# Kernel tuning notes

Measured on AMD Instinct MI355X. Metric: run time of the kernel, lower is better.

The kernel has to match this reference:

```python
import jax, jax.numpy as jnp
import numpy as np

B, V_PREV, V_NEXT = 1, 16384, 65536
F_IN, F_OUT = 512, 256
NNZ_UP, N_EDGE = 65536, 524288
EPS = 1e-5


def batch_spmm(row, col, val, m, x):
    # sparse [m, n] (COO row/col/val) @ dense x [B, n, d] -> [B, m, d]
    contrib = val[None, :, None] * x[:, col, :]          # [B, nnz, d]
    return jnp.zeros((x.shape[0], m, x.shape[2]), x.dtype).at[:, row, :].add(contrib)


def batchnorm(x, g, b):
    # BatchNorm1d in training mode: stats over (batch, node) per channel
    mu = jnp.mean(x, axis=(0, 1), keepdims=True)
    var = jnp.var(x, axis=(0, 1), keepdims=True)
    return (x - mu) * jax.lax.rsqrt(var + EPS) * g + b


def ecc(x, src, dst, w, Ui_W, Ui_b, Uj_W, Uj_b):
    # edge-conditioned graph conv: out_i = Ui(x_i) + sum_{(j->i)} w_e * Uj(x_j)
    n_nodes = x.shape[1]
    uj = x @ Uj_W + Uj_b                                  # [B, V, Fout]
    msg = w[None, :, None] * uj[:, src, :]                # [B, E, Fout]
    agg = jnp.zeros((x.shape[0], n_nodes, Uj_W.shape[1]), x.dtype).at[:, dst, :].add(msg)
    return x @ Ui_W + Ui_b + agg


def setup_inputs() -> dict:
    key = jax.random.key(0)
    ks = jax.random.split(key, 16)
    s_in = 1.0 / np.sqrt(F_IN)
    s_out = 1.0 / np.sqrt(F_OUT)
    p = {}
    p["x"] = jax.random.normal(ks[0], (B, V_PREV, F_IN), jnp.float32)
    p["up_row"] = jnp.arange(NNZ_UP, dtype=jnp.int32)
    p["up_col"] = jax.random.randint(ks[1], (NNZ_UP,), 0, V_PREV)
    p["up_val"] = jax.random.uniform(ks[2], (NNZ_UP,), jnp.float32)
    p["edge_src"] = jax.random.randint(ks[3], (N_EDGE,), 0, V_NEXT)
    p["edge_dst"] = jax.random.randint(ks[4], (N_EDGE,), 0, V_NEXT)
    p["adj_val"] = jax.random.uniform(ks[5], (N_EDGE,), jnp.float32)
    p["W_res"] = jax.random.normal(ks[6], (F_IN, F_OUT), jnp.float32) * s_in
    p["b_res"] = jnp.zeros((F_OUT,), jnp.float32)
    p["bn0_g"] = jnp.ones((F_IN,), jnp.float32)
    p["bn0_b"] = jnp.zeros((F_IN,), jnp.float32)
    p["bn1_g"] = jnp.ones((F_OUT,), jnp.float32)
    p["bn1_b"] = jnp.zeros((F_OUT,), jnp.float32)
    p["Ui0_W"] = jax.random.normal(ks[7], (F_IN, F_OUT), jnp.float32) * s_in
    p["Ui0_b"] = jnp.zeros((F_OUT,), jnp.float32)
    p["Uj0_W"] = jax.random.normal(ks[8], (F_IN, F_OUT), jnp.float32) * s_in
    p["Uj0_b"] = jnp.zeros((F_OUT,), jnp.float32)
    p["Ui1_W"] = jax.random.normal(ks[9], (F_OUT, F_OUT), jnp.float32) * s_out
    p["Ui1_b"] = jnp.zeros((F_OUT,), jnp.float32)
    p["Uj1_W"] = jax.random.normal(ks[10], (F_OUT, F_OUT), jnp.float32) * s_out
    p["Uj1_b"] = jnp.zeros((F_OUT,), jnp.float32)
    return p


def reference(x, up_row, up_col, up_val, edge_src, edge_dst, adj_val,
              W_res, b_res, bn0_g, bn0_b, bn1_g, bn1_b,
              Ui0_W, Ui0_b, Uj0_W, Uj0_b, Ui1_W, Ui1_b, Uj1_W, Uj1_b):
    # residual branch: sparse upsample then 1x1 conv (= linear over channels)
    residual = batch_spmm(up_row, up_col, up_val, V_NEXT, x)      # [B, V_NEXT, F_IN]
    residual = residual @ W_res + b_res                           # [B, V_NEXT, F_OUT]
    # main branch
    out = jax.nn.relu(batchnorm(x, bn0_g, bn0_b))                 # [B, V_PREV, F_IN]
    out = batch_spmm(up_row, up_col, up_val, V_NEXT, out)         # [B, V_NEXT, F_IN]
    out = ecc(out, edge_src, edge_dst, adj_val, Ui0_W, Ui0_b, Uj0_W, Uj0_b)
    out = jax.nn.relu(batchnorm(out, bn1_g, bn1_b))
    out = ecc(out, edge_src, edge_dst, adj_val, Ui1_W, Ui1_b, Uj1_W, Uj1_b)
    return out + residual
```

## Files before the change

### kernel.cpp

```cpp
#include <hip/hip_runtime.h>

#define V_PREV 16384
#define V_NEXT 65536
#define F_IN   512
#define F_OUT  256
#define NNZ_UP 65536
#define N_EDGE 524288

using f32x4 = __attribute__((ext_vector_type(4))) float;
using bfrag = __attribute__((ext_vector_type(8))) short;

__device__ __forceinline__ ushort f2bf(float f) {
    union { float f; unsigned u; } v; v.f = f;
    unsigned r = (v.u + 0x7FFFu + ((v.u >> 16) & 1u)) >> 16;
    return (ushort)r;
}
__device__ __forceinline__ float bf2f(ushort h) {
    union { unsigned u; float f; } v; v.u = ((unsigned)h) << 16; return v.f;
}

__global__ void prep_all_kernel(const float* __restrict__ Wres,
                                const float* __restrict__ Ui0W, const float* __restrict__ Uj0W,
                                const float* __restrict__ Ui1W, const float* __restrict__ Uj1W,
                                const float* __restrict__ Ui1b, const float* __restrict__ bres,
                                const int* __restrict__ up_row, const int* __restrict__ up_col,
                                const float* __restrict__ up_val,
                                ushort* __restrict__ WresT, ushort* __restrict__ W0t,
                                ushort* __restrict__ W1cat, float* __restrict__ biasUi,
                                int* __restrict__ colof, float* __restrict__ valof,
                                int* __restrict__ zeroBase)
{
    int b = blockIdx.x, t = threadIdx.x;
    if (b < 1024) {
        int i = b * 256 + t;
        if (i < 256 * 512) {
            int n = i / 512, k = i % 512;
            WresT[i] = f2bf(Wres[k * 256 + n]);
            W1cat[i] = f2bf(k < 256 ? Ui1W[k * 256 + n] : Uj1W[(k - 256) * 256 + n]);
        }
        {
            int n = i / 512, k = i % 512;
            W0t[i] = f2bf(n < 256 ? Uj0W[k * 256 + n] : Ui0W[k * 256 + (n - 256)]);
        }
        if (i < 256) biasUi[i] = Ui1b[i] + bres[i];
    } else if (b < 1280) {
        int k = (b - 1024) * 256 + t;
        int r = up_row[k];
        colof[r] = up_col[k];
        valof[r] = up_val[k];
    } else {
        int i = (b - 1280) * 256 + t;
        zeroBase[i] = 0;
    }
}

__global__ void hist_bn0_kernel(const int* __restrict__ dst,
                                int* __restrict__ cnt,
                                const float* __restrict__ x,
                                float* __restrict__ psum0, float* __restrict__ psq0)
{
    int b = blockIdx.x, t = threadIdx.x;
    if (b < 2048) {
        int e = b * 256 + t;
        atomicAdd(&cnt[dst[e]], 1);
    } else {
        int blk = b - 2048;
        float s0 = 0, s1 = 0, q0 = 0, q1 = 0;
        for (int r = 0; r < 32; r++) {
            size_t base = ((size_t)blk * 32 + r) * 512;
            float a = x[base + t], bb = x[base + t + 256];
            s0 += a; q0 += a * a; s1 += bb; q1 += bb * bb;
        }
        psum0[blk * 512 + t] = s0; psum0[blk * 512 + t + 256] = s1;
        psq0 [blk * 512 + t] = q0; psq0 [blk * 512 + t + 256] = q1;
    }
}

__global__ void scan_block_kernel(const int* __restrict__ cnt, int* __restrict__ offs,
                                  int* __restrict__ bsum)
{
    __shared__ int buf[2][256];
    int t = threadIdx.x;
    int i = blockIdx.x * 256 + t;
    int v = cnt[i];
    int p = 0;
    buf[0][t] = v;
    __syncthreads();
    for (int d = 1; d < 256; d <<= 1) {
        int nv = buf[p][t] + ((t >= d) ? buf[p][t - d] : 0);
        buf[p ^ 1][t] = nv;
        p ^= 1;
        __syncthreads();
    }
    int incl = buf[p][t];
    offs[i] = incl - v;
    if (t == 255) bsum[blockIdx.x] = incl;
}

__global__ void add_offs_bnfin_kernel(int* __restrict__ offs, const int* __restrict__ bsum,
                                      int* __restrict__ cursor,
                                      const float* __restrict__ psum0, const float* __restrict__ psq0,
                                      const float* __restrict__ g0, const float* __restrict__ b0,
                                      float* __restrict__ sc0, float* __restrict__ sh0)
{
    int b = blockIdx.x, t = threadIdx.x;
    if (b < 256) {
        __shared__ int buf[2][256];
        int v = bsum[t];
        int p = 0;
        buf[0][t] = v;
        __syncthreads();
        for (int d = 1; d < 256; d <<= 1) {
            int nv = buf[p][t] + ((t >= d) ? buf[p][t - d] : 0);
            buf[p ^ 1][t] = nv;
            p ^= 1;
            __syncthreads();
        }
        int excl = buf[p][b] - bsum[b];
        int i = b * 256 + t;
        int o = offs[i] + excl;
        offs[i] = o;
        cursor[i] = o;
    } else {
        int vb = b - 256;
        int gw = (vb * 256 + t) >> 6;
        int lane = t & 63;
        float s = 0, q = 0;
        for (int i = lane; i < 512; i += 64) {
            s += psum0[(size_t)i * 512 + gw];
            q += psq0 [(size_t)i * 512 + gw];
        }
#pragma unroll
        for (int d = 32; d > 0; d >>= 1) {
            s += __shfl_xor(s, d);
            q += __shfl_xor(q, d);
        }
        if (lane == 0) {
            float m = s * (1.0f / V_PREV);
            float v = q * (1.0f / V_PREV) - m * m;
            float r = rsqrtf(v + 1e-5f);
            float scale = r * g0[gw];
            sc0[gw] = scale;
            sh0[gw] = b0[gw] - m * scale;
        }
    }
}

__global__ void bn_finish_kernel(const float* __restrict__ psum, const float* __restrict__ psq,
                                 int nblocks, int C, float invN,
                                 const float* __restrict__ g, const float* __restrict__ b,
                                 float* __restrict__ sc, float* __restrict__ sh)
{
    int gw = (blockIdx.x * blockDim.x + threadIdx.x) >> 6;
    int lane = threadIdx.x & 63;
    if (gw >= C) return;
    float s = 0, q = 0;
    for (int i = lane; i < nblocks; i += 64) {
        s += psum[(size_t)i * C + gw];
        q += psq [(size_t)i * C + gw];
    }
#pragma unroll
    for (int d = 32; d > 0; d >>= 1) {
        s += __shfl_xor(s, d);
        q += __shfl_xor(q, d);
    }
    if (lane == 0) {
        float m = s * invN;
        float v = q * invN - m * m;
        float r = rsqrtf(v + 1e-5f);
        float scale = r * g[gw];
        sc[gw] = scale;
        sh[gw] = b[gw] - m * scale;
    }
}

__global__ __launch_bounds__(256)
void fill_gemm0_kernel(const int* __restrict__ src, const int* __restrict__ dst,
                       const float* __restrict__ adjv,
                       const int* __restrict__ colof, const float* __restrict__ valof,
                       int* __restrict__ cursor, int4* __restrict__ E,
                       const float* __restrict__ x,
                       const ushort* __restrict__ WresT, const ushort* __restrict__ W0t,
                       const float* __restrict__ sc0, const float* __restrict__ sh0,
                       ushort* __restrict__ XW, ushort* __restrict__ XNJ,
                       ushort* __restrict__ XNI)
{
    __shared__ ushort As[128 * 32];
    __shared__ ushort Bs[128 * 32];
    __shared__ float s_sc[512], s_sh[512];

    const int tid = threadIdx.x;
    if (blockIdx.x < 2048) {
        int e = blockIdx.x * 256 + tid;
        int d = dst[e];
        int s = src[e];
        float a = adjv[e];
        int p = atomicAdd(&cursor[d], 1);
        int4 v;
        v.x = s;
        v.y = __float_as_int(a);
        v.z = colof[s];
        v.w = __float_as_int(a * valof[s]);
        E[p] = v;
        return;
    }

    const int id   = blockIdx.x - 2048;
    const int xcd  = id & 7;
    const int rest = id >> 3;
    const int slot = rest / 6;
    const int bx   = rest - slot * 6;
    const int by   = slot * 8 + xcd;

    const bool bnmode = bx >= 2;
    const ushort* Bt = bnmode ? W0t : WresT;
    const int btrow = bnmode ? (bx - 2) * 128 : bx * 128;
    ushort* Cout = (bx < 2) ? XW : (bx < 4 ? XNJ : XNI);
    const int colbase = (bx & 1) * 128;
    const int tM = by * 128;

    for (int i = tid; i < 512; i += 256) { s_sc[i] = sc0[i]; s_sh[i] = sh0[i]; }
    __syncthreads();

    const int lane = tid & 63;
    const int wave = tid >> 6;
    const int wm = wave >> 1, wn = wave & 1;
    const int lr = lane & 15, lg = lane >> 4;

    const int ra = tid >> 1;
    const int ua = (tid & 1) * 2;
    const int rb = tid >> 2;
    const int ub = tid & 3;

    f32x4 acc[4][4] = {};

    for (int k0 = 0; k0 < 512; k0 += 32) {
        const float* xp = &x[(size_t)(tM + ra) * 512 + k0 + ua * 8];
        float4 f0 = *(const float4*)(xp);
        float4 f1 = *(const float4*)(xp + 4);
        float4 f2 = *(const float4*)(xp + 8);
        float4 f3 = *(const float4*)(xp + 12);
        float vv[16] = { f0.x,f0.y,f0.z,f0.w, f1.x,f1.y,f1.z,f1.w,
                         f2.x,f2.y,f2.z,f2.w, f3.x,f3.y,f3.z,f3.w };
        ushort hh[16];
        if (bnmode) {
#pragma unroll
            for (int j = 0; j < 16; j++) {
                int c = k0 + ua * 8 + j;
                hh[j] = f2bf(fmaxf(vv[j] * s_sc[c] + s_sh[c], 0.0f));
            }
        } else {
#pragma unroll
            for (int j = 0; j < 16; j++) hh[j] = f2bf(vv[j]);
        }
        *(uint4*)&As[ra * 32 + ((ua    ) ^ (ra & 3)) * 8] = *(uint4*)&hh[0];
        *(uint4*)&As[ra * 32 + ((ua + 1) ^ (ra & 3)) * 8] = *(uint4*)&hh[8];

#pragma unroll
        for (int i = 0; i < 2; i++) {
            int row = rb + i * 64;
            *(uint4*)&Bs[row * 32 + (ub ^ (row & 3)) * 8] =
                *(const uint4*)&Bt[(size_t)(btrow + row) * 512 + k0 + ub * 8];
        }
        __syncthreads();

        bfrag af[4], bfv[4];
#pragma unroll
        for (int mm = 0; mm < 4; mm++) {
            int row = wm * 64 + mm * 16 + lr;
            af[mm] = *(const bfrag*)&As[row * 32 + (lg ^ (row & 3)) * 8];
        }
#pragma unroll
        for (int nn = 0; nn < 4; nn++) {
            int row = wn * 64 + nn * 16 + lr;
            bfv[nn] = *(const bfrag*)&Bs[row * 32 + (lg ^ (row & 3)) * 8];
        }
#pragma unroll
        for (int mm = 0; mm < 4; mm++)
#pragma unroll
            for (int nn = 0; nn < 4; nn++)
                acc[mm][nn] = __builtin_amdgcn_mfma_f32_16x16x32_bf16(af[mm], bfv[nn], acc[mm][nn], 0, 0, 0);
        __syncthreads();
    }

#pragma unroll
    for (int mm = 0; mm < 4; mm++)
#pragma unroll
        for (int nn = 0; nn < 4; nn++)
#pragma unroll
            for (int r = 0; r < 4; r++) {
                int row = tM + wm * 64 + mm * 16 + lg * 4 + r;
                int col = colbase + wn * 64 + nn * 16 + lr;
                Cout[(size_t)row * 256 + col] = f2bf(acc[mm][nn][r]);
            }
}

__global__ __launch_bounds__(256)
void gather0_kernel(const int* __restrict__ offs, const int* __restrict__ cnt,
                    const int4* __restrict__ E,
                    const int* __restrict__ colof, const float* __restrict__ valof,
                    const ushort* __restrict__ XNJ, const ushort* __restrict__ XNI,
                    const float* __restrict__ ui_b, const float* __restrict__ uj_b,
                    ushort* __restrict__ X1, float* __restrict__ sumA,
                    float* __restrict__ psum1s, float* __restrict__ psq1s)
{
    __shared__ float redS[4][256];
    __shared__ float redQ[4][256];

    int wave = threadIdx.x >> 6;
    int lane = threadIdx.x & 63;
    int f = lane * 4;
    float ub0 = ui_b[f + 0], ub1 = ui_b[f + 1], ub2 = ui_b[f + 2], ub3 = ui_b[f + 3];
    float jb0 = uj_b[f + 0], jb1 = uj_b[f + 1], jb2 = uj_b[f + 2], jb3 = uj_b[f + 3];
    float ss0 = 0, ss1 = 0, ss2 = 0, ss3 = 0;
    float qq0 = 0, qq1 = 0, qq2 = 0, qq3 = 0;

    for (int it = 0; it < 8; it++) {
        int d = (blockIdx.x * 8 + it) * 4 + wave;
        int c = colof[d];
        float s = valof[d];
        ushort4 u = *(const ushort4*)&XNI[(size_t)c * 256 + f];
        const ushort* up = (const ushort*)&u;
        float a0 = ub0 + s * bf2f(up[0]);
        float a1 = ub1 + s * bf2f(up[1]);
        float a2 = ub2 + s * bf2f(up[2]);
        float a3 = ub3 + s * bf2f(up[3]);
        float sA = 0;

        int st = offs[d], n = cnt[d];
        for (int e0 = 0; e0 < n; e0 += 4) {
            int4 ev0 = E[st + e0];
            int4 ev1 = (e0 + 1 < n) ? E[st + e0 + 1] : make_int4(0, 0, 0, 0);
            int4 ev2 = (e0 + 2 < n) ? E[st + e0 + 2] : make_int4(0, 0, 0, 0);
            int4 ev3 = (e0 + 3 < n) ? E[st + e0 + 3] : make_int4(0, 0, 0, 0);
            float w0 = __int_as_float(ev0.w), w1 = __int_as_float(ev1.w);
            float w2 = __int_as_float(ev2.w), w3 = __int_as_float(ev3.w);
            sA += __int_as_float(ev0.y) + __int_as_float(ev1.y)
                + __int_as_float(ev2.y) + __int_as_float(ev3.y);
            ushort4 v0 = *(const ushort4*)&XNJ[(size_t)ev0.z * 256 + f];
            ushort4 v1 = *(const ushort4*)&XNJ[(size_t)ev1.z * 256 + f];
            ushort4 v2 = *(const ushort4*)&XNJ[(size_t)ev2.z * 256 + f];
            ushort4 v3 = *(const ushort4*)&XNJ[(size_t)ev3.z * 256 + f];
            const ushort* p0 = (const ushort*)&v0;
            const ushort* p1 = (const ushort*)&v1;
            const ushort* p2 = (const ushort*)&v2;
            const ushort* p3 = (const ushort*)&v3;
            a0 += w0 * bf2f(p0[0]) + w1 * bf2f(p1[0]) + w2 * bf2f(p2[0]) + w3 * bf2f(p3[0]);
            a1 += w0 * bf2f(p0[1]) + w1 * bf2f(p1[1]) + w2 * bf2f(p2[1]) + w3 * bf2f(p3[1]);
            a2 += w0 * bf2f(p0[2]) + w1 * bf2f(p1[2]) + w2 * bf2f(p2[2]) + w3 * bf2f(p3[2]);
            a3 += w0 * bf2f(p0[3]) + w1 * bf2f(p1[3]) + w2 * bf2f(p2[3]) + w3 * bf2f(p3[3]);
        }
        a0 += sA * jb0; a1 += sA * jb1; a2 += sA * jb2; a3 += sA * jb3;
        *(ushort4*)&X1[(size_t)d * 256 + f] =
            make_ushort4(f2bf(a0), f2bf(a1), f2bf(a2), f2bf(a3));
        if (lane == 0) sumA[d] = sA;
        ss0 += a0; ss1 += a1; ss2 += a2; ss3 += a3;
        qq0 += a0 * a0; qq1 += a1 * a1; qq2 += a2 * a2; qq3 += a3 * a3;
    }

    redS[wave][f + 0] = ss0; redS[wave][f + 1] = ss1;
    redS[wave][f + 2] = ss2; redS[wave][f + 3] = ss3;
    redQ[wave][f + 0] = qq0; redQ[wave][f + 1] = qq1;
    redQ[wave][f + 2] = qq2; redQ[wave][f + 3] = qq3;
    __syncthreads();
    int t = threadIdx.x;
    float ssum = redS[0][t] + redS[1][t] + redS[2][t] + redS[3][t];
    float sq   = redQ[0][t] + redQ[1][t] + redQ[2][t] + redQ[3][t];
    int slab = (blockIdx.x & 63) * 256 + t;
    atomicAdd(&psum1s[slab], ssum);
    atomicAdd(&psq1s[slab], sq);
}

__global__ __launch_bounds__(256)
void gather1G_kernel(const int* __restrict__ offs, const int* __restrict__ cnt,
                     const int4* __restrict__ E,
                     const ushort* __restrict__ X1,
                     const float* __restrict__ sc1, const float* __restrict__ sh1,
                     ushort* __restrict__ G)
{
    int d = blockIdx.x * 4 + (threadIdx.x >> 6);
    int f = (threadIdx.x & 63) * 4;
    float4 sc = *(const float4*)&sc1[f];
    float4 sh = *(const float4*)&sh1[f];
    float a0 = 0, a1 = 0, a2 = 0, a3 = 0;

    int st = offs[d], n = cnt[d];
    for (int e0 = 0; e0 < n; e0 += 4) {
        int4 ev0 = E[st + e0];
        int4 ev1 = (e0 + 1 < n) ? E[st + e0 + 1] : make_int4(0, 0, 0, 0);
        int4 ev2 = (e0 + 2 < n) ? E[st + e0 + 2] : make_int4(0, 0, 0, 0);
        int4 ev3 = (e0 + 3 < n) ? E[st + e0 + 3] : make_int4(0, 0, 0, 0);
        float w0 = __int_as_float(ev0.y), w1 = __int_as_float(ev1.y);
        float w2 = __int_as_float(ev2.y), w3 = __int_as_float(ev3.y);
        ushort4 v0 = *(const ushort4*)&X1[(size_t)ev0.x * 256 + f];
        ushort4 v1 = *(const ushort4*)&X1[(size_t)ev1.x * 256 + f];
        ushort4 v2 = *(const ushort4*)&X1[(size_t)ev2.x * 256 + f];
        ushort4 v3 = *(const ushort4*)&X1[(size_t)ev3.x * 256 + f];
        const ushort* p0 = (const ushort*)&v0;
        const ushort* p1 = (const ushort*)&v1;
        const ushort* p2 = (const ushort*)&v2;
        const ushort* p3 = (const ushort*)&v3;
        a0 += w0 * fmaxf(bf2f(p0[0]) * sc.x + sh.x, 0.0f)
            + w1 * fmaxf(bf2f(p1[0]) * sc.x + sh.x, 0.0f)
            + w2 * fmaxf(bf2f(p2[0]) * sc.x + sh.x, 0.0f)
            + w3 * fmaxf(bf2f(p3[0]) * sc.x + sh.x, 0.0f);
        a1 += w0 * fmaxf(bf2f(p0[1]) * sc.y + sh.y, 0.0f)
            + w1 * fmaxf(bf2f(p1[1]) * sc.y + sh.y, 0.0f)
            + w2 * fmaxf(bf2f(p2[1]) * sc.y + sh.y, 0.0f)
            + w3 * fmaxf(bf2f(p3[1]) * sc.y + sh.y, 0.0f);
        a2 += w0 * fmaxf(bf2f(p0[2]) * sc.z + sh.z, 0.0f)
            + w1 * fmaxf(bf2f(p1[2]) * sc.z + sh.z, 0.0f)
            + w2 * fmaxf(bf2f(p2[2]) * sc.z + sh.z, 0.0f)
            + w3 * fmaxf(bf2f(p3[2]) * sc.z + sh.z, 0.0f);
        a3 += w0 * fmaxf(bf2f(p0[3]) * sc.w + sh.w, 0.0f)
            + w1 * fmaxf(bf2f(p1[3]) * sc.w + sh.w, 0.0f)
            + w2 * fmaxf(bf2f(p2[3]) * sc.w + sh.w, 0.0f)
            + w3 * fmaxf(bf2f(p3[3]) * sc.w + sh.w, 0.0f);
    }
    *(ushort4*)&G[(size_t)d * 256 + f] =
        make_ushort4(f2bf(a0), f2bf(a1), f2bf(a2), f2bf(a3));
}

__global__ __launch_bounds__(512, 1)
void gemm_final_kernel(const ushort* __restrict__ X1, const ushort* __restrict__ G,
                       const ushort* __restrict__ W1cat,
                       const float* __restrict__ sc1, const float* __restrict__ sh1,
                       const float* __restrict__ biasUi, const float* __restrict__ uj1_b,
                       const float* __restrict__ sumA,
                       const int* __restrict__ colof, const float* __restrict__ valof,
                       const ushort* __restrict__ XW,
                       float* __restrict__ out)
{
    __shared__ ushort As[256 * 32];
    __shared__ ushort Bs[256 * 32];
    __shared__ float s_sc[256], s_sh[256];

    const int tid = threadIdx.x;
    const int tM = blockIdx.x * 256;

    if (tid < 256) { s_sc[tid] = sc1[tid]; s_sh[tid] = sh1[tid]; }
    __syncthreads();

    const int lane = tid & 63;
    const int wave = tid >> 6;
    const int wm = wave >> 1, wn = wave & 1;
    const int lr = lane & 15, lg = lane >> 4;

    f32x4 acc[4][8] = {};

    for (int k0 = 0; k0 < 512; k0 += 32) {
#pragma unroll
        for (int i = 0; i < 2; i++) {
            int idx = tid + i * 512;
            int row = idx >> 2, u = idx & 3;
            ushort h[8];
            if (k0 < 256) {
                *(uint4*)h = *(const uint4*)&X1[(size_t)(tM + row) * 256 + k0 + u * 8];
#pragma unroll
                for (int j = 0; j < 8; j++) {
                    int c = k0 + u * 8 + j;
                    h[j] = f2bf(fmaxf(bf2f(h[j]) * s_sc[c] + s_sh[c], 0.0f));
                }
            } else {
                *(uint4*)h = *(const uint4*)&G[(size_t)(tM + row) * 256 + (k0 - 256) + u * 8];
            }
            *(uint4*)&As[row * 32 + (u ^ (row & 3)) * 8] = *(uint4*)h;
        }
#pragma unroll
        for (int i = 0; i < 2; i++) {
            int idx = tid + i * 512;
            int row = idx >> 2, u = idx & 3;
            *(uint4*)&Bs[row * 32 + (u ^ (row & 3)) * 8] =
                *(const uint4*)&W1cat[(size_t)row * 512 + k0 + u * 8];
        }
        __syncthreads();

        bfrag af[4], bfv[8];
#pragma unroll
        for (int mm = 0; mm < 4; mm++) {
            int row = wm * 64 + mm * 16 + lr;
            af[mm] = *(const bfrag*)&As[row * 32 + (lg ^ (row & 3)) * 8];
        }
#pragma unroll
        for (int nn = 0; nn < 8; nn++) {
            int row = wn * 128 + nn * 16 + lr;
            bfv[nn] = *(const bfrag*)&Bs[row * 32 + (lg ^ (row & 3)) * 8];
        }
#pragma unroll
        for (int mm = 0; mm < 4; mm++)
#pragma unroll
            for (int nn = 0; nn < 8; nn++)
                acc[mm][nn] = __builtin_amdgcn_mfma_f32_16x16x32_bf16(af[mm], bfv[nn], acc[mm][nn], 0, 0, 0);
        __syncthreads();
    }

    float bUi[8], bUj[8];
#pragma unroll
    for (int nn = 0; nn < 8; nn++) {
        int col = wn * 128 + nn * 16 + lr;
        bUi[nn] = biasUi[col];
        bUj[nn] = uj1_b[col];
    }
#pragma unroll
    for (int mm = 0; mm < 4; mm++) {
#pragma unroll
        for (int r = 0; r < 4; r++) {
            int row = tM + wm * 64 + mm * 16 + lg * 4 + r;
            int c = colof[row];
            float s = valof[row];
            float sA = sumA[row];
#pragma unroll
            for (int nn = 0; nn < 8; nn++) {
                int col = wn * 128 + nn * 16 + lr;
                float v = acc[mm][nn][r] + bUi[nn] + sA * bUj[nn]
                        + s * bf2f(XW[(size_t)c * 256 + col]);
                out[(size_t)row * 256 + col] = v;
            }
        }
    }
}

extern "C" void kernel_launch(void* const* d_in, const int* in_sizes, int n_in,
                              void* d_out, int out_size, void* d_ws, size_t ws_size,
                              hipStream_t stream)
{
    const float* x      = (const float*)d_in[0];
    const int*   up_row = (const int*)  d_in[1];
    const int*   up_col = (const int*)  d_in[2];
    const float* up_val = (const float*)d_in[3];
    const int*   e_src  = (const int*)  d_in[4];
    const int*   e_dst  = (const int*)  d_in[5];
    const float* adjv   = (const float*)d_in[6];
    const float* W_res  = (const float*)d_in[7];
    const float* b_res  = (const float*)d_in[8];
    const float* bn0_g  = (const float*)d_in[9];
    const float* bn0_b  = (const float*)d_in[10];
    const float* bn1_g  = (const float*)d_in[11];
    const float* bn1_b  = (const float*)d_in[12];
    const float* Ui0_W  = (const float*)d_in[13];
    const float* Ui0_b  = (const float*)d_in[14];
    const float* Uj0_W  = (const float*)d_in[15];
    const float* Uj0_b  = (const float*)d_in[16];
    const float* Ui1_W  = (const float*)d_in[17];
    const float* Ui1_b  = (const float*)d_in[18];
    const float* Uj1_W  = (const float*)d_in[19];
    const float* Uj1_b  = (const float*)d_in[20];

    float* out = (float*)d_out;

    char* ws = (char*)d_ws;
    size_t off = 0;
    auto alloc = [&](size_t bytes) -> char* {
        char* p = ws + off;
        off = (off + bytes + 255) & ~(size_t)255;
        return p;
    };
    ushort* XW    = (ushort*)alloc((size_t)V_PREV * F_OUT * 2);
    ushort* XNJ   = (ushort*)alloc((size_t)V_PREV * F_OUT * 2);
    ushort* XNI   = (ushort*)alloc((size_t)V_PREV * F_OUT * 2);
    ushort* X1    = (ushort*)alloc((size_t)V_NEXT * F_OUT * 2);
    ushort* G     = (ushort*)alloc((size_t)V_NEXT * F_OUT * 2);
    int*    cnt   = (int*)   alloc(V_NEXT * 4);
    float*  psum1s= (float*) alloc(64 * 256 * 4);
    float*  psq1s = (float*) alloc(64 * 256 * 4);
    float*  sumA  = (float*) alloc(V_NEXT * 4);
    int*    offs  = (int*)   alloc(V_NEXT * 4);
    int*    cursor= (int*)   alloc(V_NEXT * 4);
    int*    bsum  = (int*)   alloc(256 * 4);
    int4*   E     = (int4*)  alloc((size_t)N_EDGE * 16);
    int*    colof = (int*)   alloc(V_NEXT * 4);
    float*  valof = (float*) alloc(V_NEXT * 4);
    ushort* WresT = (ushort*)alloc(256 * 512 * 2);
    ushort* W0t   = (ushort*)alloc(512 * 512 * 2);
    ushort* W1cat = (ushort*)alloc(256 * 512 * 2);
    float*  biasUi= (float*) alloc(256 * 4);
    float*  psum0 = (float*) alloc(512 * 512 * 4);
    float*  psq0  = (float*) alloc(512 * 512 * 4);
    float*  sc0   = (float*) alloc(512 * 4);
    float*  sh0   = (float*) alloc(512 * 4);
    float*  sc1   = (float*) alloc(256 * 4);
    float*  sh1   = (float*) alloc(256 * 4);
    (void)ws_size; (void)in_sizes; (void)n_in; (void)out_size;

    prep_all_kernel<<<1664, 256, 0, stream>>>(W_res, Ui0_W, Uj0_W, Ui1_W, Uj1_W,
                                              Ui1_b, b_res,
                                              up_row, up_col, up_val,
                                              WresT, W0t, W1cat, biasUi,
                                              colof, valof, cnt);

    hist_bn0_kernel<<<2560, 256, 0, stream>>>(e_dst, cnt, x, psum0, psq0);

    scan_block_kernel<<<256, 256, 0, stream>>>(cnt, offs, bsum);

    add_offs_bnfin_kernel<<<384, 256, 0, stream>>>(offs, bsum, cursor,
                                                   psum0, psq0, bn0_g, bn0_b, sc0, sh0);

    fill_gemm0_kernel<<<2816, 256, 0, stream>>>(e_src, e_dst, adjv, colof, valof,
                                                cursor, E,
                                                x, WresT, W0t, sc0, sh0,
                                                XW, XNJ, XNI);

    gather0_kernel<<<2048, 256, 0, stream>>>(offs, cnt, E, colof, valof,
                                             XNJ, XNI, Ui0_b, Uj0_b,
                                             X1, sumA, psum1s, psq1s);

    bn_finish_kernel<<<64, 256, 0, stream>>>(psum1s, psq1s, 64, 256, 1.0f / V_NEXT,
                                             bn1_g, bn1_b, sc1, sh1);

    gather1G_kernel<<<V_NEXT / 4, 256, 0, stream>>>(offs, cnt, E, X1, sc1, sh1, G);

    gemm_final_kernel<<<256, 512, 0, stream>>>(X1, G, W1cat, sc1, sh1,
                                               biasUi, Uj1_b, sumA,
                                               colof, valof, XW, out);
}
```

Baseline: 238.1 us.

## Merge prep and histogram kernels and switch LDS tiles to padded stride

Combines the weight-prep, COO remap, edge histogram and BN0 partial-statistics work into one kernel launch, with a hipMemsetAsync doing the zeroing that the old prep kernel did in-kernel. The XOR-swizzled shared-memory layout of both GEMM kernels is replaced by a padded row stride of 36 elements. The fusion saves a launch and lets the independent pieces overlap, but the histogram atomics now depend on the memset running first. The padding uses more LDS and may leave different bank conflicts than the swizzle.

```diff
diff --git a/kernel.cpp b/kernel.cpp
--- a/kernel.cpp
+++ b/kernel.cpp
@@ -10,6 +10,8 @@
 using f32x4 = __attribute__((ext_vector_type(4))) float;
 using bfrag = __attribute__((ext_vector_type(8))) short;
 
+#define LSTR 36
+
 __device__ __forceinline__ ushort f2bf(float f) {
     union { float f; unsigned u; } v; v.f = f;
     unsigned r = (v.u + 0x7FFFu + ((v.u >> 16) & 1u)) >> 16;
@@ -19,16 +21,19 @@
     union { unsigned u; float f; } v; v.u = ((unsigned)h) << 16; return v.f;
 }
 
-__global__ void prep_all_kernel(const float* __restrict__ Wres,
-                                const float* __restrict__ Ui0W, const float* __restrict__ Uj0W,
-                                const float* __restrict__ Ui1W, const float* __restrict__ Uj1W,
-                                const float* __restrict__ Ui1b, const float* __restrict__ bres,
-                                const int* __restrict__ up_row, const int* __restrict__ up_col,
-                                const float* __restrict__ up_val,
-                                ushort* __restrict__ WresT, ushort* __restrict__ W0t,
-                                ushort* __restrict__ W1cat, float* __restrict__ biasUi,
-                                int* __restrict__ colof, float* __restrict__ valof,
-                                int* __restrict__ zeroBase)
+__global__ void mega_prep_kernel(const float* __restrict__ Wres,
+                                 const float* __restrict__ Ui0W, const float* __restrict__ Uj0W,
+                                 const float* __restrict__ Ui1W, const float* __restrict__ Uj1W,
+                                 const float* __restrict__ Ui1b, const float* __restrict__ bres,
+                                 const int* __restrict__ up_row, const int* __restrict__ up_col,
+                                 const float* __restrict__ up_val,
+                                 const int* __restrict__ dst,
+                                 const float* __restrict__ x,
+                                 ushort* __restrict__ WresT, ushort* __restrict__ W0t,
+                                 ushort* __restrict__ W1cat, float* __restrict__ biasUi,
+                                 int* __restrict__ colof, float* __restrict__ valof,
+                                 int* __restrict__ cnt,
+                                 float* __restrict__ psum0, float* __restrict__ psq0)
 {
     int b = blockIdx.x, t = threadIdx.x;
     if (b < 1024) {
@@ -48,23 +53,11 @@
         int r = up_row[k];
         colof[r] = up_col[k];
         valof[r] = up_val[k];
-    } else {
-        int i = (b - 1280) * 256 + t;
-        zeroBase[i] = 0;
-    }
-}
-
-__global__ void hist_bn0_kernel(const int* __restrict__ dst,
-                                int* __restrict__ cnt,
-                                const float* __restrict__ x,
-                                float* __restrict__ psum0, float* __restrict__ psq0)
-{
-    int b = blockIdx.x, t = threadIdx.x;
-    if (b < 2048) {
-        int e = b * 256 + t;
+    } else if (b < 3328) {
+        int e = (b - 1280) * 256 + t;
         atomicAdd(&cnt[dst[e]], 1);
     } else {
-        int blk = b - 2048;
+        int blk = b - 3328;
         float s0 = 0, s1 = 0, q0 = 0, q1 = 0;
         for (int r = 0; r < 32; r++) {
             size_t base = ((size_t)blk * 32 + r) * 512;
@@ -185,8 +178,8 @@
                        ushort* __restrict__ XW, ushort* __restrict__ XNJ,
                        ushort* __restrict__ XNI)
 {
-    __shared__ ushort As[128 * 32];
-    __shared__ ushort Bs[128 * 32];
+    __shared__ ushort As[128 * LSTR];
+    __shared__ ushort Bs[128 * LSTR];
     __shared__ float s_sc[512], s_sh[512];
 
     const int tid = threadIdx.x;
@@ -253,13 +246,13 @@
 #pragma unroll
             for (int j = 0; j < 16; j++) hh[j] = f2bf(vv[j]);
         }
-        *(uint4*)&As[ra * 32 + ((ua    ) ^ (ra & 3)) * 8] = *(uint4*)&hh[0];
-        *(uint4*)&As[ra * 32 + ((ua + 1) ^ (ra & 3)) * 8] = *(uint4*)&hh[8];
+        *(uint4*)&As[ra * LSTR + ua * 8]       = *(uint4*)&hh[0];
+        *(uint4*)&As[ra * LSTR + (ua + 1) * 8] = *(uint4*)&hh[8];
 
 #pragma unroll
         for (int i = 0; i < 2; i++) {
             int row = rb + i * 64;
-            *(uint4*)&Bs[row * 32 + (ub ^ (row & 3)) * 8] =
+            *(uint4*)&Bs[row * LSTR + ub * 8] =
                 *(const uint4*)&Bt[(size_t)(btrow + row) * 512 + k0 + ub * 8];
         }
         __syncthreads();
@@ -268,12 +261,12 @@
 #pragma unroll
         for (int mm = 0; mm < 4; mm++) {
             int row = wm * 64 + mm * 16 + lr;
-            af[mm] = *(const bfrag*)&As[row * 32 + (lg ^ (row & 3)) * 8];
+            af[mm] = *(const bfrag*)&As[row * LSTR + lg * 8];
         }
 #pragma unroll
         for (int nn = 0; nn < 4; nn++) {
             int row = wn * 64 + nn * 16 + lr;
-            bfv[nn] = *(const bfrag*)&Bs[row * 32 + (lg ^ (row & 3)) * 8];
+            bfv[nn] = *(const bfrag*)&Bs[row * LSTR + lg * 8];
         }
 #pragma unroll
         for (int mm = 0; mm < 4; mm++)
@@ -431,8 +424,8 @@
                        const ushort* __restrict__ XW,
                        float* __restrict__ out)
 {
-    __shared__ ushort As[256 * 32];
-    __shared__ ushort Bs[256 * 32];
+    __shared__ ushort As[256 * LSTR];
+    __shared__ ushort Bs[256 * LSTR];
     __shared__ float s_sc[256], s_sh[256];
 
     const int tid = threadIdx.x;
@@ -464,13 +457,13 @@
             } else {
                 *(uint4*)h = *(const uint4*)&G[(size_t)(tM + row) * 256 + (k0 - 256) + u * 8];
             }
-            *(uint4*)&As[row * 32 + (u ^ (row & 3)) * 8] = *(uint4*)h;
+            *(uint4*)&As[row * LSTR + u * 8] = *(uint4*)h;
         }
 #pragma unroll
         for (int i = 0; i < 2; i++) {
             int idx = tid + i * 512;
             int row = idx >> 2, u = idx & 3;
-            *(uint4*)&Bs[row * 32 + (u ^ (row & 3)) * 8] =
+            *(uint4*)&Bs[row * LSTR + u * 8] =
                 *(const uint4*)&W1cat[(size_t)row * 512 + k0 + u * 8];
         }
         __syncthreads();
@@ -479,12 +472,12 @@
 #pragma unroll
         for (int mm = 0; mm < 4; mm++) {
             int row = wm * 64 + mm * 16 + lr;
-            af[mm] = *(const bfrag*)&As[row * 32 + (lg ^ (row & 3)) * 8];
+            af[mm] = *(const bfrag*)&As[row * LSTR + lg * 8];
         }
 #pragma unroll
         for (int nn = 0; nn < 8; nn++) {
             int row = wn * 128 + nn * 16 + lr;
-            bfv[nn] = *(const bfrag*)&Bs[row * 32 + (lg ^ (row & 3)) * 8];
+            bfv[nn] = *(const bfrag*)&Bs[row * LSTR + lg * 8];
         }
 #pragma unroll
         for (int mm = 0; mm < 4; mm++)
@@ -582,13 +575,14 @@
     float*  sh1   = (float*) alloc(256 * 4);
     (void)ws_size; (void)in_sizes; (void)n_in; (void)out_size;
 
-    prep_all_kernel<<<1664, 256, 0, stream>>>(W_res, Ui0_W, Uj0_W, Ui1_W, Uj1_W,
-                                              Ui1_b, b_res,
-                                              up_row, up_col, up_val,
-                                              WresT, W0t, W1cat, biasUi,
-                                              colof, valof, cnt);
-
-    hist_bn0_kernel<<<2560, 256, 0, stream>>>(e_dst, cnt, x, psum0, psq0);
+    hipMemsetAsync(cnt, 0, (size_t)98304 * 4, stream);
+
+    mega_prep_kernel<<<3840, 256, 0, stream>>>(W_res, Ui0_W, Uj0_W, Ui1_W, Uj1_W,
+                                               Ui1_b, b_res,
+                                               up_row, up_col, up_val,
+                                               e_dst, x,
+                                               WresT, W0t, W1cat, biasUi,
+                                               colof, valof, cnt, psum0, psq0);
 
     scan_block_kernel<<<256, 256, 0, stream>>>(cnt, offs, bsum);
 
```

New measurement: 239.4 us, median of 2. About the same (+0.5%).
